# Kernel optimization log

Hardware: AMD Instinct MI355X
Metric: run time of the kernel (lower is better)

The kernel has to match this reference:

```python
import jax, jax.numpy as jnp
import numpy as np

WIN_SIZE = 16
STRIDE = 8
H = W = 512
B = 8
C = 3


def gaussian_blend(win_size):
    # matches WindowOverlapProcessor._create_gaussian_weights
    sigma = win_size / 4.0
    x = jnp.arange(win_size, dtype=jnp.float32) - (win_size - 1) / 2.0
    g = jnp.exp(-(x ** 2) / (2.0 * sigma ** 2))
    g = g / g.sum()
    return g[:, None] * g[None, :]  # [ws, ws]


def setup_inputs() -> dict:
    key = jax.random.key(0)
    hw = (H - WIN_SIZE) // STRIDE + 1  # 63
    ww = (W - WIN_SIZE) // STRIDE + 1  # 63
    nw = hw * ww  # 3969
    hs = (jnp.arange(hw) * STRIDE).astype(jnp.int64 if jax.config.jax_enable_x64 else jnp.int32)
    ws_ = (jnp.arange(ww) * STRIDE).astype(hs.dtype)
    coords = jnp.stack(
        [jnp.repeat(hs, ww), jnp.tile(ws_, hw)], axis=-1
    )  # [nw, 2] regular overlapping grid
    windows = jax.random.normal(key, (B, nw, WIN_SIZE, WIN_SIZE, C), dtype=jnp.float32)
    return {
        "windows": windows,
        "window_coords": coords,
        "h_windows": hw,
        "w_windows": ww,
        "stride": STRIDE,
        "original_h": H,
        "original_w": W,
        "channels": C,
    }


def reference(windows, window_coords, h_windows, w_windows, stride,
              original_h, original_w, channels):
    Bb, nw, ws, _, Cc = windows.shape
    blend = gaussian_blend(ws)  # [ws, ws]

    # flat pixel index for every window element
    dh = jnp.arange(ws)
    dw = jnp.arange(ws)
    offs = dh[:, None] * original_w + dw[None, :]            # [ws, ws]
    base = window_coords[:, 0] * original_w + window_coords[:, 1]  # [nw]
    idx = (base[:, None, None] + offs[None]).reshape(-1)     # [nw*ws*ws]

    # weighted window values, [B, C, nw*ws*ws]
    contrib = windows * blend[None, None, :, :, None]
    contrib = contrib.transpose(0, 4, 1, 2, 3).reshape(Bb, Cc, -1)

    recon = jnp.zeros((Bb, Cc, original_h * original_w), windows.dtype)
    recon = recon.at[:, :, idx].add(contrib)

    wsum = jnp.zeros((original_h * original_w,), blend.dtype)
    wsum = wsum.at[idx].add(jnp.tile(blend.reshape(-1), nw))

    recon = recon / (wsum[None, None, :] + 1e-8)
    return recon.reshape(Bb, Cc, original_h, original_w)
```

## Files before the change

### kernel.cpp

```cpp
#include <hip/hip_runtime.h>


#define OH 512
#define OW 512
#define NB 8
#define NC 3
#define HWIN 63
#define NWIN (HWIN * HWIN)
#define PLANE (OH * OW)

typedef float f4 __attribute__((ext_vector_type(4)));

__device__ __forceinline__ float gblend(int d) {
    const float x = (float)d - 7.5f;
    return __expf(-(x * x) * 0.03125f) * 0.1044284f;
}

__device__ __forceinline__ float getf(const f4 (&a)[3], int f) {
    return a[f >> 2][f & 3];
}

__global__ __launch_bounds__(256) void window_overlap_kernel(
    const float* __restrict__ win, float* __restrict__ out) {
    const int g = blockIdx.x * 256 + threadIdx.x;
    const int w0 = (g & 127) << 2;
    const int h = (g >> 7) & (OH - 1);
    const int b = g >> 16;

    const int i1 = min(h >> 3, HWIN - 1);
    const int dh1 = h - i1 * 8;
    const int i0 = max(i1 - 1, 0);
    const int dh0 = (dh1 <= 7) ? dh1 + 8 : dh1;
    const float gh1 = gblend(dh1);
    const float gh0 = (i1 >= 1 && dh1 <= 7) ? gblend(dh0) : 0.0f;

    const int j = w0 >> 3;
    const int c0 = w0 & 7;
    const int jB = min(j, HWIN - 1);
    const int jA = max(j - 1, 0);
    const float fB = (j <= HWIN - 1) ? 1.0f : 0.0f;
    const float fA = (j >= 1) ? 1.0f : 0.0f;

    const f4* __restrict__ w4 = (const f4*)win;
    const int sB = (c0 >> 2) * 3;
    const int rb = b * NWIN;
    const int oA0 = (rb + i0 * HWIN + jA) * 192 + dh0 * 12 + sB + 6;
    const int oB0 = (rb + i0 * HWIN + jB) * 192 + dh0 * 12 + sB;
    const int oA1 = (rb + i1 * HWIN + jA) * 192 + dh1 * 12 + sB + 6;
    const int oB1 = (rb + i1 * HWIN + jB) * 192 + dh1 * 12 + sB;

    f4 A0[3], B0[3], A1[3], B1[3];
#pragma unroll
    for (int k = 0; k < 3; ++k) A0[k] = w4[oA0 + k];
#pragma unroll
    for (int k = 0; k < 3; ++k) B0[k] = w4[oB0 + k];
#pragma unroll
    for (int k = 0; k < 3; ++k) A1[k] = w4[oA1 + k];
#pragma unroll
    for (int k = 0; k < 3; ++k) B1[k] = w4[oB1 + k];

    const f4 wB = c0 ? (f4){0.0712141f, 0.0859006f, 0.0973380f, 0.1036157f}
                     : (f4){0.0180058f, 0.0278880f, 0.0405766f, 0.0554615f};
    const f4 wA = c0 ? (f4){0.0554615f, 0.0405766f, 0.0278880f, 0.0180058f}
                     : (f4){0.1036157f, 0.0973380f, 0.0859006f, 0.0712141f};

    const float ghs = gh0 + gh1;
    f4 o[NC];
#pragma unroll
    for (int k = 0; k < 4; ++k) {
        const float wBk = fB * wB[k];
        const float wAk = fA * wA[k];
        const float r = __builtin_amdgcn_rcpf(ghs * (wAk + wBk) + 1e-8f);
        const float aA0 = wAk * gh0, aA1 = wAk * gh1;
        const float aB0 = wBk * gh0, aB1 = wBk * gh1;
#pragma unroll
        for (int ch = 0; ch < NC; ++ch) {
            const int f = 3 * k + ch;
            const float v = aA0 * getf(A0, f) + aB0 * getf(B0, f) +
                            aA1 * getf(A1, f) + aB1 * getf(B1, f);
            o[ch][k] = v * r;
        }
    }

    const int p = b * (NC * PLANE) + h * OW + w0;
    __builtin_nontemporal_store(o[0], (f4*)&out[p]);
    __builtin_nontemporal_store(o[1], (f4*)&out[p + PLANE]);
    __builtin_nontemporal_store(o[2], (f4*)&out[p + 2 * PLANE]);
}

extern "C" void kernel_launch(void* const* d_in, const int* in_sizes, int n_in,
                              void* d_out, int out_size, void* d_ws, size_t ws_size,
                              hipStream_t stream) {
    const float* windows = (const float*)d_in[0];
    float* out = (float*)d_out;
    window_overlap_kernel<<<2048, 256, 0, stream>>>(windows, out);
}
```

Baseline: 163.8 us.

## Stage window half-rows in LDS per 8-row band tile before blending

```diff
diff --git a/kernel.cpp b/kernel.cpp
--- a/kernel.cpp
+++ b/kernel.cpp
@@ -8,6 +8,10 @@
 #define HWIN 63
 #define NWIN (HWIN * HWIN)
 #define PLANE (OH * OW)
+#define CH_F4 96
+#define CH_PAD 97
+#define NCHUNK 34
+#define NF4 (NCHUNK * CH_F4)
 
 typedef float f4 __attribute__((ext_vector_type(4)));
 
@@ -20,69 +24,80 @@
     return a[f >> 2][f & 3];
 }
 
-__global__ __launch_bounds__(256) void window_overlap_kernel(
+__global__ __launch_bounds__(256, 3) void window_overlap_kernel(
     const float* __restrict__ win, float* __restrict__ out) {
-    const int g = blockIdx.x * 256 + threadIdx.x;
-    const int w0 = (g & 127) << 2;
-    const int h = (g >> 7) & (OH - 1);
-    const int b = g >> 16;
+    __shared__ f4 lds[NCHUNK * CH_PAD];
 
-    const int i1 = min(h >> 3, HWIN - 1);
-    const int dh1 = h - i1 * 8;
-    const int i0 = max(i1 - 1, 0);
-    const int dh0 = (dh1 <= 7) ? dh1 + 8 : dh1;
-    const float gh1 = gblend(dh1);
-    const float gh0 = (i1 >= 1 && dh1 <= 7) ? gblend(dh0) : 0.0f;
+    const int tid = threadIdx.x;
+    const int bi = blockIdx.x;
+    const int t = bi & 3;
+    const int q = (bi >> 2) & 63;
+    const int b = bi >> 8;
 
-    const int j = w0 >> 3;
-    const int c0 = w0 & 7;
-    const int jB = min(j, HWIN - 1);
-    const int jA = max(j - 1, 0);
-    const float fB = (j <= HWIN - 1) ? 1.0f : 0.0f;
-    const float fA = (j >= 1) ? 1.0f : 0.0f;
+    const int qL = min(q, 62);
+    const int qH = max(q - 1, 0);
+    const int bOff = b * NWIN;
 
     const f4* __restrict__ w4 = (const f4*)win;
-    const int sB = (c0 >> 2) * 3;
-    const int rb = b * NWIN;
-    const int oA0 = (rb + i0 * HWIN + jA) * 192 + dh0 * 12 + sB + 6;
-    const int oB0 = (rb + i0 * HWIN + jB) * 192 + dh0 * 12 + sB;
-    const int oA1 = (rb + i1 * HWIN + jA) * 192 + dh1 * 12 + sB + 6;
-    const int oB1 = (rb + i1 * HWIN + jB) * 192 + dh1 * 12 + sB;
+#pragma unroll
+    for (int ii = 0; ii < 13; ++ii) {
+        const int flat = ii * 256 + tid;
+        if (flat < NF4) {
+            const int c = flat / CH_F4;
+            const int e = flat - c * CH_F4;
+            const int hi = (c >= 17) ? 1 : 0;
+            const int k = c - hi * 17;
+            const int jj = min(max(16 * t - 1 + k, 0), HWIN - 1);
+            const int qr = hi ? qH : qL;
+            const int base = (bOff + qr * HWIN + jj) * 192 + hi * CH_F4;
+            lds[c * CH_PAD + e] = w4[base + e];
+        }
+    }
+    __syncthreads();
 
-    f4 A0[3], B0[3], A1[3], B1[3];
+    const int r = tid >> 5;
+    const int w4p = (tid & 31) << 2;
+    const int jl = w4p >> 3;
+    const int c0 = w4p & 7;
+    const int jg = 16 * t + jl;
+    const float fB = (jg <= HWIN - 1) ? 1.0f : 0.0f;
+    const float fA = (jg >= 1) ? 1.0f : 0.0f;
+    const float wT = (q <= 62) ? gblend(r) : 0.0f;
+    const float wB = (q >= 1) ? gblend(r + 8) : 0.0f;
+
+    const int s0 = (c0 >> 2) * 3;
+    const int rowf = r * 12;
+    const f4* LoB = &lds[(jl + 1) * CH_PAD + rowf + s0];
+    const f4* LoA = &lds[jl * CH_PAD + rowf + 6 + s0];
+    const f4* HiB = &lds[(17 + jl + 1) * CH_PAD + rowf + s0];
+    const f4* HiA = &lds[(17 + jl) * CH_PAD + rowf + 6 + s0];
+    f4 lb[3], la[3], hb[3], ha[3];
 #pragma unroll
-    for (int k = 0; k < 3; ++k) A0[k] = w4[oA0 + k];
+    for (int k = 0; k < 3; ++k) { lb[k] = LoB[k]; la[k] = LoA[k]; }
 #pragma unroll
-    for (int k = 0; k < 3; ++k) B0[k] = w4[oB0 + k];
-#pragma unroll
-    for (int k = 0; k < 3; ++k) A1[k] = w4[oA1 + k];
-#pragma unroll
-    for (int k = 0; k < 3; ++k) B1[k] = w4[oB1 + k];
+    for (int k = 0; k < 3; ++k) { hb[k] = HiB[k]; ha[k] = HiA[k]; }
 
-    const f4 wB = c0 ? (f4){0.0712141f, 0.0859006f, 0.0973380f, 0.1036157f}
+    const f4 gB = c0 ? (f4){0.0712141f, 0.0859006f, 0.0973380f, 0.1036157f}
                      : (f4){0.0180058f, 0.0278880f, 0.0405766f, 0.0554615f};
-    const f4 wA = c0 ? (f4){0.0554615f, 0.0405766f, 0.0278880f, 0.0180058f}
+    const f4 gA = c0 ? (f4){0.0554615f, 0.0405766f, 0.0278880f, 0.0180058f}
                      : (f4){0.1036157f, 0.0973380f, 0.0859006f, 0.0712141f};
 
-    const float ghs = gh0 + gh1;
     f4 o[NC];
 #pragma unroll
-    for (int k = 0; k < 4; ++k) {
-        const float wBk = fB * wB[k];
-        const float wAk = fA * wA[k];
-        const float r = __builtin_amdgcn_rcpf(ghs * (wAk + wBk) + 1e-8f);
-        const float aA0 = wAk * gh0, aA1 = wAk * gh1;
-        const float aB0 = wBk * gh0, aB1 = wBk * gh1;
+    for (int m = 0; m < 4; ++m) {
+        const float wBc = fB * gB[m];
+        const float wAc = fA * gA[m];
+        const float rn = __builtin_amdgcn_rcpf((wT + wB) * (wAc + wBc) + 1e-8f);
 #pragma unroll
         for (int ch = 0; ch < NC; ++ch) {
-            const int f = 3 * k + ch;
-            const float v = aA0 * getf(A0, f) + aB0 * getf(B0, f) +
-                            aA1 * getf(A1, f) + aB1 * getf(B1, f);
-            o[ch][k] = v * r;
+            const int f = 3 * m + ch;
+            const float v = wT * (wAc * getf(la, f) + wBc * getf(lb, f)) +
+                            wB * (wAc * getf(ha, f) + wBc * getf(hb, f));
+            o[ch][m] = v * rn;
         }
     }
 
-    const int p = b * (NC * PLANE) + h * OW + w0;
+    const int p = b * (NC * PLANE) + (8 * q + r) * OW + 128 * t + w4p;
     __builtin_nontemporal_store(o[0], (f4*)&out[p]);
     __builtin_nontemporal_store(o[1], (f4*)&out[p + PLANE]);
     __builtin_nontemporal_store(o[2], (f4*)&out[p + 2 * PLANE]);
```

New measurement: 163.6 us. No clear change (-0.1%).
